# Kernel tuning notes

Measured on AMD Instinct MI355X. Metric: run time of the kernel, lower is better.

The kernel has to match this reference:

```python
import jax, jax.numpy as jnp
import numpy as np

B = 16384       # batch
H = 512         # hidden_size
OUT = 4         # output_size (== GRU input_size)
FF = 2048       # MLP hidden width
HORIZON = 5     # prediction_horizon


def setup_inputs() -> dict:
    key = jax.random.key(0)
    ks = jax.random.split(key, 12)
    s = 0.05
    f32 = jnp.float32
    return {
        "predicted_values": jax.random.normal(ks[0], (B, HORIZON, OUT), f32),
        "past_time_features": jax.random.normal(ks[1], (B, H), f32),
        # nn.GRU (single layer) params, PyTorch layout: (3H, in) / (3H, H), gate order r,z,n
        "w_ih": jax.random.normal(ks[2], (3 * H, OUT), f32) * s,
        "w_hh": jax.random.normal(ks[3], (3 * H, H), f32) * s,
        "b_ih": jax.random.normal(ks[4], (3 * H,), f32) * s,
        "b_hh": jax.random.normal(ks[5], (3 * H,), f32) * s,
        # hx_fc: Linear(2H -> H)
        "w_fc": jax.random.normal(ks[6], (H, 2 * H), f32) * s,
        "b_fc": jax.random.normal(ks[7], (H,), f32) * s,
        # mlp: Linear(H -> 2048), Linear(2048 -> OUT); Dropout is identity at eval
        "w1": jax.random.normal(ks[8], (FF, H), f32) * s,
        "b1": jax.random.normal(ks[9], (FF,), f32) * s,
        "w2": jax.random.normal(ks[10], (OUT, FF), f32) * s,
        "b2": jax.random.normal(ks[11], (OUT,), f32) * s,
    }


def _gru_cell(x, h, w_ih, w_hh, b_ih, b_hh):
    # PyTorch GRU cell: gates ordered (r, z, n)
    gi = x @ w_ih.T + b_ih          # [B, 3H]
    gh = h @ w_hh.T + b_hh          # [B, 3H]
    i_r, i_z, i_n = jnp.split(gi, 3, axis=-1)
    h_r, h_z, h_n = jnp.split(gh, 3, axis=-1)
    r = jax.nn.sigmoid(i_r + h_r)
    z = jax.nn.sigmoid(i_z + h_z)
    n = jnp.tanh(i_n + r * h_n)
    return (1.0 - z) * n + z * h


def reference(predicted_values, past_time_features, w_ih, w_hh, b_ih, b_hh,
              w_fc, b_fc, w1, b1, w2, b2):
    b = predicted_values.shape[0]
    xy = jnp.zeros((b, OUT), predicted_values.dtype)
    hx = past_time_features.reshape(b, H)
    outs = []
    for i in range(HORIZON):
        # length-2 sequence through the GRU: [xy, predicted_values[:, i]]
        h1 = _gru_cell(xy, hx, w_ih, w_hh, b_ih, b_hh)
        h2 = _gru_cell(predicted_values[:, i, :], h1, w_ih, w_hh, b_ih, b_hh)
        hcat = jnp.concatenate([h1, h2], axis=-1)        # [B, 2H]
        hx = hcat @ w_fc.T + b_fc                        # [B, H]
        # MLP: ReLU -> Linear -> (Dropout=identity) -> ReLU -> Linear
        d_xy = jax.nn.relu(jax.nn.relu(hx) @ w1.T + b1) @ w2.T + b2
        xy = xy + d_xy
        outs.append(xy)
    return jnp.stack(outs, axis=1)                       # [B, HORIZON, OUT]
```

## Files before the change

### kernel.cpp

```cpp
#include <hip/hip_runtime.h>
#include <hip/hip_bf16.h>
#include <cstdint>
#include <cstddef>

#define Bsz 16384
#define HORsz 5

using bf16_t = __hip_bfloat16;
typedef __bf16 bf16x8 __attribute__((ext_vector_type(8)));
typedef float f32x4 __attribute__((ext_vector_type(4)));

__device__ __forceinline__ void gld_lds16(const void* g, void* l) {
  __builtin_amdgcn_global_load_lds((__attribute__((address_space(1))) void*)g,
                                   (__attribute__((address_space(3))) void*)l,
                                   16, 0, 0);
}

__device__ __forceinline__ float sigm(float x) { return 1.f / (1.f + __expf(-x)); }
__device__ __forceinline__ float tanh_fast(float x) {
  x = fminf(fmaxf(x, -20.f), 20.f);
  float e = __expf(2.f * x);
  return (e - 1.f) / (e + 1.f);
}

__device__ __forceinline__ void swz(int b, int nbn, int& n, int& m) {
  const int x = b & 7;
  const int k = b >> 3;
  n = k % nbn;
  m = x + 8 * (k / nbn);
}

__device__ __forceinline__ size_t fl_off(int row, int col, int ca, int cofs) {
  return (size_t)((row >> 4) * ca + cofs + (col >> 5)) * 1024
       + (size_t)((((col >> 3) & 3) * 16 + (row & 15)) * 16 + (col & 7) * 2);
}

__global__ void __launch_bounds__(256) pack_fl(const float* __restrict__ src,
                                               char* __restrict__ dst,
                                               int C, int cs, int npieces) {
  const int p = blockIdx.x * 256 + threadIdx.x;
  if (p >= npieces) return;
  const int chunk = p >> 6, wi = p & 63;
  const int colgrp = wi >> 4, r15 = wi & 15;
  const int rowgrp = chunk >> cs, kg = chunk & ((1 << cs) - 1);
  const int row = rowgrp * 16 + r15;
  const int col = kg * 32 + colgrp * 8;
  const float* s = src + (size_t)row * C + col;
  bf16x8 v;
  #pragma unroll
  for (int j = 0; j < 8; ++j) v[j] = (__bf16)s[j];
  *(bf16x8*)(dst + (size_t)p * 16) = v;
}

__global__ void __launch_bounds__(256, 3) gru_fused4(
    const char* __restrict__ Afl, int ca,
    const char* __restrict__ Wfl,
    const float* __restrict__ x, int ldx,
    const float* __restrict__ w_ih, const float* __restrict__ b_ih,
    const float* __restrict__ b_hh,
    char* __restrict__ Ofl, int co, int kofs)
{
  __shared__ char smem[32768];
  const int t = threadIdx.x, w = t >> 6, lane = t & 63;
  int bn, bm;
  swz(blockIdx.x, 8, bn, bm);
  const int m0 = bm * 64;
  const int n0 = bn * 64;

  const char* gsrc[4];
  int loff[4];
  #pragma unroll
  for (int s = 0; s < 4; ++s) {
    const int idx = w * 4 + s;
    if (idx < 4) {
      gsrc[s] = Afl + (size_t)((m0 >> 4) + idx) * ca * 1024 + lane * 16;
    } else {
      const int c = idx - 4, g = c >> 2, cr = c & 3;
      gsrc[s] = Wfl + (size_t)(g * 32 + (n0 >> 4) + cr) * 16 * 1024 + lane * 16;
    }
    loff[s] = idx * 1024;
  }

  f32x4 acc[3][4];
  const f32x4 zero = {0.f, 0.f, 0.f, 0.f};
  #pragma unroll
  for (int g = 0; g < 3; ++g)
    #pragma unroll
    for (int i = 0; i < 4; ++i) acc[g][i] = zero;

  #pragma unroll
  for (int s = 0; s < 4; ++s)
    gld_lds16(gsrc[s], smem + loff[s]);

  #pragma unroll
  for (int kg = 0; kg < 16; ++kg) {
    __syncthreads();
    const char* cur = smem + (kg & 1) * 16384;
    if (kg + 1 < 16) {
      char* nxt = smem + ((kg + 1) & 1) * 16384;
      #pragma unroll
      for (int s = 0; s < 4; ++s)
        gld_lds16(gsrc[s] + (size_t)(kg + 1) * 1024, nxt + loff[s]);
    }
    bf16x8 af[4];
    #pragma unroll
    for (int i = 0; i < 4; ++i)
      af[i] = *(const bf16x8*)(cur + i * 1024 + lane * 16);
    #pragma unroll
    for (int g = 0; g < 3; ++g) {
      const bf16x8 bv = *(const bf16x8*)(cur + (4 + g * 4 + w) * 1024 + lane * 16);
      #pragma unroll
      for (int i = 0; i < 4; ++i)
        acc[g][i] = __builtin_amdgcn_mfma_f32_16x16x32_bf16(af[i], bv, acc[g][i], 0, 0, 0);
    }
  }

  const int lr = lane & 15, q4 = (lane >> 4) * 4;
  char* rep = smem + w * 2048;
  const int c = n0 + w * 16 + lr;
  const float4 wr  = *(const float4*)(w_ih + (size_t)c * 4);
  const float4 wz  = *(const float4*)(w_ih + (size_t)(c + 512) * 4);
  const float4 wnn = *(const float4*)(w_ih + (size_t)(c + 1024) * 4);
  const float bir = b_ih[c], biz = b_ih[c + 512], bin = b_ih[c + 1024];
  const float bhr = b_hh[c], bhz = b_hh[c + 512], bhn = b_hh[c + 1024];
  const int wbase = ((lr >> 3) * 16 + q4) * 16 + (lr & 7) * 2;
  #pragma unroll
  for (int i = 0; i < 4; ++i) {
    #pragma unroll
    for (int r4 = 0; r4 < 4; ++r4) {
      const int row = m0 + i * 16 + q4 + r4;
      const float4 xv = *(const float4*)(x + (size_t)row * ldx);
      const float gir = bir + xv.x * wr.x  + xv.y * wr.y  + xv.z * wr.z  + xv.w * wr.w;
      const float giz = biz + xv.x * wz.x  + xv.y * wz.y  + xv.z * wz.z  + xv.w * wz.w;
      const float gin = bin + xv.x * wnn.x + xv.y * wnn.y + xv.z * wnn.z + xv.w * wnn.w;
      const float rr = sigm(gir + acc[0][i][r4] + bhr);
      const float zz = sigm(giz + acc[1][i][r4] + bhz);
      const float nn = tanh_fast(gin + rr * (acc[2][i][r4] + bhn));
      const float hp = (float)*(const __bf16*)(Afl + fl_off(row, c, ca, 0));
      *(__bf16*)(rep + i * 512 + wbase + r4 * 16) = (__bf16)((1.f - zz) * nn + zz * hp);
    }
  }
  const int rg0 = m0 >> 4;
  const int cg = kofs + (n0 >> 5) + (w >> 1);
  const int half = (w & 1) * 512;
  #pragma unroll
  for (int i = 0; i < 4; ++i) {
    const uint2 v = *(const uint2*)(rep + i * 512 + lane * 8);
    *(uint2*)(Ofl + ((size_t)(rg0 + i) * co + cg) * 1024 + half + lane * 8) = v;
  }
}

template <int NKG, int NJ, int MODE>
__global__ void __launch_bounds__(256, 4) gemm_fl5(
    const char* __restrict__ Afl,
    const char* __restrict__ Bfl, int nbn,
    const float* __restrict__ bias,
    char* __restrict__ O1, char* __restrict__ O2, int co,
    const float* __restrict__ w2, float* __restrict__ dxy)
{
  constexpr int NCH = 8 + 2 * NJ;
  constexpr int NS = NCH / 4;
  constexpr int BUFB = NCH * 1024;
  __shared__ char smem[2 * BUFB];
  const int t = threadIdx.x, w = t >> 6, lane = t & 63;
  int bn, bm;
  swz(blockIdx.x, nbn, bn, bm);
  const int m0 = bm * 128, n0 = bn * (NJ * 32);
  const int wm = (w >> 1) * 64, wn = (w & 1) * (NJ * 16);

  const char* gsrc[NS];
  int loff[NS];
  #pragma unroll
  for (int s = 0; s < NS; ++s) {
    const int idx = w * NS + s;
    if (idx < 8) gsrc[s] = Afl + (size_t)((m0 >> 4) + idx) * NKG * 1024 + lane * 16;
    else         gsrc[s] = Bfl + (size_t)((n0 >> 4) + idx - 8) * NKG * 1024 + lane * 16;
    loff[s] = idx * 1024;
  }

  f32x4 acc[4][NJ];
  const f32x4 zero = {0.f, 0.f, 0.f, 0.f};
  #pragma unroll
  for (int i = 0; i < 4; ++i)
    #pragma unroll
    for (int j = 0; j < NJ; ++j) acc[i][j] = zero;

  #pragma unroll
  for (int s = 0; s < NS; ++s)
    gld_lds16(gsrc[s], smem + loff[s]);

  #pragma unroll
  for (int kg = 0; kg < NKG; ++kg) {
    __syncthreads();
    const char* cur = smem + (kg & 1) * BUFB;
    if (kg + 1 < NKG) {
      char* nxt = smem + ((kg + 1) & 1) * BUFB;
      #pragma unroll
      for (int s = 0; s < NS; ++s)
        gld_lds16(gsrc[s] + (size_t)(kg + 1) * 1024, nxt + loff[s]);
    }
    bf16x8 af[4], bv[NJ];
    #pragma unroll
    for (int i = 0; i < 4; ++i)
      af[i] = *(const bf16x8*)(cur + ((wm >> 4) + i) * 1024 + lane * 16);
    #pragma unroll
    for (int j = 0; j < NJ; ++j)
      bv[j] = *(const bf16x8*)(cur + (8 + (wn >> 4) + j) * 1024 + lane * 16);
    #pragma unroll
    for (int i = 0; i < 4; ++i)
      #pragma unroll
      for (int j = 0; j < NJ; ++j)
        acc[i][j] = __builtin_amdgcn_mfma_f32_16x16x32_bf16(af[i], bv[j], acc[i][j], 0, 0, 0);
  }

  const int lr = lane & 15, q4 = (lane >> 4) * 4;
  if (MODE == 2) {
    char* rep = smem + w * (NJ / 2) * 1024;
    const int rgb = (m0 >> 4) + (wm >> 4);
    const int cgb = (n0 >> 5) + (wn >> 5);
    for (int i = 0; i < 4; ++i) {
      #pragma unroll
      for (int j = 0; j < NJ; ++j) {
        const int col = n0 + wn + j * 16 + lr;
        const float bvv = bias[col];
        const int wbase = (((j & 1) * 2 + (lr >> 3)) * 16 + q4) * 16 + (lr & 7) * 2;
        #pragma unroll
        for (int r = 0; r < 4; ++r) {
          const float v = acc[i][j][r] + bvv;
          *(__bf16*)(rep + (j >> 1) * 1024 + wbase + r * 16) = (__bf16)v;
        }
      }
      #pragma unroll
      for (int jc = 0; jc < NJ / 2; ++jc) {
        const bf16x8 v = *(const bf16x8*)(rep + jc * 1024 + lane * 16);
        const size_t cb = ((size_t)(rgb + i) * co + cgb + jc) * 1024 + lane * 16;
        *(bf16x8*)(O1 + cb) = v;
        bf16x8 vr;
        #pragma unroll
        for (int e = 0; e < 8; ++e) vr[e] = (__bf16)fmaxf((float)v[e], 0.f);
        *(bf16x8*)(O2 + cb) = vr;
      }
    }
  }
}

__global__ void __launch_bounds__(512, 2) mlp2b(
    const char* __restrict__ Afl,
    const char* __restrict__ Bfl,
    const float* __restrict__ bias,
    const float* __restrict__ w2,
    float* __restrict__ dxy)
{
  __shared__ char smem[2 * 32768];
  const int t = threadIdx.x, w = t >> 6, lane = t & 63;
  const int wr = w >> 2, wc = w & 3;
  int bn, bm;
  swz(blockIdx.x, 8, bn, bm);
  const int m0 = bm * 256, n0 = bn * 256;

  const char* gsrc[4];
  int loff[4];
  #pragma unroll
  for (int s = 0; s < 4; ++s) {
    const int idx = w * 4 + s;
    if (idx < 16) {
      gsrc[s] = Afl + (size_t)((m0 >> 4) + idx) * 16 * 1024 + lane * 16;
      loff[s] = idx * 1024;
    } else {
      gsrc[s] = Bfl + (size_t)((n0 >> 4) + idx - 16) * 16 * 1024 + lane * 16;
      loff[s] = 16384 + (idx - 16) * 1024;
    }
  }

  f32x4 acc[8][4];
  const f32x4 zero = {0.f, 0.f, 0.f, 0.f};
  #pragma unroll
  for (int i = 0; i < 8; ++i)
    #pragma unroll
    for (int j = 0; j < 4; ++j) acc[i][j] = zero;

  #pragma unroll
  for (int s = 0; s < 4; ++s)
    gld_lds16(gsrc[s], smem + loff[s]);

  #pragma unroll
  for (int kg = 0; kg < 16; ++kg) {
    __syncthreads();
    const char* cur = smem + (kg & 1) * 32768;
    if (kg + 1 < 16) {
      char* nxt = smem + ((kg + 1) & 1) * 32768;
      #pragma unroll
      for (int s = 0; s < 4; ++s)
        gld_lds16(gsrc[s] + (size_t)(kg + 1) * 1024, nxt + loff[s]);
    }
    bf16x8 af[8], bv[4];
    #pragma unroll
    for (int j = 0; j < 4; ++j)
      bv[j] = *(const bf16x8*)(cur + 16384 + (wc * 4 + j) * 1024 + lane * 16);
    #pragma unroll
    for (int i = 0; i < 8; ++i)
      af[i] = *(const bf16x8*)(cur + (wr * 8 + i) * 1024 + lane * 16);
    __builtin_amdgcn_s_setprio(1);
    #pragma unroll
    for (int i = 0; i < 8; ++i)
      #pragma unroll
      for (int j = 0; j < 4; ++j)
        acc[i][j] = __builtin_amdgcn_mfma_f32_16x16x32_bf16(af[i], bv[j], acc[i][j], 0, 0, 0);
    __builtin_amdgcn_s_setprio(0);
  }

  const int lr = lane & 15, q4 = (lane >> 4) * 4;
  const int slice = bn * 4 + wc;
  #pragma unroll
  for (int i = 0; i < 8; ++i) {
    float v[4][4];
    #pragma unroll
    for (int r = 0; r < 4; ++r)
      #pragma unroll
      for (int o = 0; o < 4; ++o) v[r][o] = 0.f;
    #pragma unroll
    for (int j = 0; j < 4; ++j) {
      const int col = n0 + wc * 64 + j * 16 + lr;
      const float bvv = bias[col];
      const float w20 = w2[col], w21 = w2[2048 + col], w22 = w2[4096 + col], w23 = w2[6144 + col];
      #pragma unroll
      for (int r = 0; r < 4; ++r) {
        const float pv = fmaxf(acc[i][j][r] + bvv, 0.f);
        v[r][0] += pv * w20; v[r][1] += pv * w21; v[r][2] += pv * w22; v[r][3] += pv * w23;
      }
    }
    #pragma unroll
    for (int m = 1; m <= 8; m <<= 1)
      #pragma unroll
      for (int r = 0; r < 4; ++r)
        #pragma unroll
        for (int o = 0; o < 4; ++o) v[r][o] += __shfl_xor(v[r][o], m);
    if (lr == 0) {
      #pragma unroll
      for (int r = 0; r < 4; ++r) {
        const int row = m0 + wr * 128 + i * 16 + q4 + r;
        float4 vv = make_float4(v[r][0], v[r][1], v[r][2], v[r][3]);
        *(float4*)(dxy + ((size_t)slice * Bsz + row) * 4) = vv;
      }
    }
  }
}

__global__ void __launch_bounds__(256) finalize(
    const float* __restrict__ dxy, const float* __restrict__ b2,
    float* __restrict__ xy, float* __restrict__ out, int istep)
{
  const int b = blockIdx.x * 256 + threadIdx.x;
  float4 s = *(const float4*)b2;
  #pragma unroll 8
  for (int sl = 0; sl < 32; ++sl) {
    const float4 d = *(const float4*)(dxy + ((size_t)sl * Bsz + b) * 4);
    s.x += d.x; s.y += d.y; s.z += d.z; s.w += d.w;
  }
  float4 xv = *(const float4*)(xy + (size_t)b * 4);
  xv.x += s.x; xv.y += s.y; xv.z += s.z; xv.w += s.w;
  *(float4*)(xy + (size_t)b * 4) = xv;
  *(float4*)(out + (size_t)b * 20 + istep * 4) = xv;
}

extern "C" void kernel_launch(void* const* d_in, const int* in_sizes, int n_in,
                              void* d_out, int out_size, void* d_ws, size_t ws_size,
                              hipStream_t stream)
{
  const float* pv   = (const float*)d_in[0];
  const float* ptf  = (const float*)d_in[1];
  const float* w_ih = (const float*)d_in[2];
  const float* w_hh = (const float*)d_in[3];
  const float* b_ih = (const float*)d_in[4];
  const float* b_hh = (const float*)d_in[5];
  const float* w_fc = (const float*)d_in[6];
  const float* b_fc = (const float*)d_in[7];
  const float* w1   = (const float*)d_in[8];
  const float* b1   = (const float*)d_in[9];
  const float* w2   = (const float*)d_in[10];
  const float* b2   = (const float*)d_in[11];
  float* out = (float*)d_out;

  char* p = (char*)d_ws;
  auto carve = [&](size_t bytes) {
    char* r = p;
    p += (bytes + 255) & ~(size_t)255;
    return r;
  };
  char*  hxF   = carve((size_t)Bsz * 512 * 2);
  char*  hxrF  = carve((size_t)Bsz * 512 * 2);
  char*  hcatF = carve((size_t)Bsz * 1024 * 2);
  float* dxy   = (float*)carve((size_t)32 * Bsz * 4 * 4);
  float* xy    = (float*)carve((size_t)Bsz * 4 * 4);
  char*  whhF  = carve((size_t)1536 * 512 * 2);
  char*  wfcF  = carve((size_t)512 * 1024 * 2);
  char*  w1F   = carve((size_t)2048 * 512 * 2);

  pack_fl<<<(1536 * 512 / 8 + 255) / 256, 256, 0, stream>>>(w_hh, whhF, 512, 4, 1536 * 512 / 8);
  pack_fl<<<(512 * 1024 / 8 + 255) / 256, 256, 0, stream>>>(w_fc, wfcF, 1024, 5, 512 * 1024 / 8);
  pack_fl<<<(2048 * 512 / 8 + 255) / 256, 256, 0, stream>>>(w1, w1F, 512, 4, 2048 * 512 / 8);
  pack_fl<<<(Bsz * 512 / 8 + 255) / 256, 256, 0, stream>>>(ptf, hxF, 512, 4, Bsz * 512 / 8);
  hipMemsetAsync(xy, 0, (size_t)Bsz * 4 * 4, stream);

  for (int i = 0; i < HORsz; ++i) {
    gru_fused4<<<2048, 256, 0, stream>>>(
        hxF, 16, whhF, xy, 4, w_ih, b_ih, b_hh, hcatF, 32, 0);
    gru_fused4<<<2048, 256, 0, stream>>>(
        hcatF, 32, whhF, pv + i * 4, HORsz * 4, w_ih, b_ih, b_hh, hcatF, 32, 16);
    gemm_fl5<32, 4, 2><<<512, 256, 0, stream>>>(
        hcatF, wfcF, 4, b_fc, hxF, hxrF, 16, nullptr, nullptr);
    mlp2b<<<512, 512, 0, stream>>>(hxrF, w1F, b1, w2, dxy);
    finalize<<<Bsz / 256, 256, 0, stream>>>(dxy, b2, xy, out, i);
  }
}
```

Baseline: 876.5 us.

## Double GRU tile rows to 128, hoist MLP epilogue loads, use DPP reductions

The GRU kernel tile grows from 64 to 128 batch rows per block, so each W_hh chunk loaded into shared memory feeds twice as many MFMAs. The grid is halved, shared memory and accumulator registers grow, and launch bounds drop to 2 blocks per SM. In the MLP epilogue, bias and w2 loads are hoisted out of the row loop. The 16-lane shuffle reduction is replaced with DPP adds. The risk is lower occupancy and register pressure in the GRU kernel.

```diff
diff --git a/kernel.cpp b/kernel.cpp
--- a/kernel.cpp
+++ b/kernel.cpp
@@ -21,6 +21,19 @@
   x = fminf(fmaxf(x, -20.f), 20.f);
   float e = __expf(2.f * x);
   return (e - 1.f) / (e + 1.f);
+}
+
+template <int CTRL>
+__device__ __forceinline__ float dpp_add(float v) {
+  int x = __builtin_amdgcn_update_dpp(0, __float_as_int(v), CTRL, 0xF, 0xF, true);
+  return v + __int_as_float(x);
+}
+__device__ __forceinline__ float red16(float v) {
+  v = dpp_add<0xB1>(v);
+  v = dpp_add<0x4E>(v);
+  v = dpp_add<0x124>(v);
+  v = dpp_add<0x128>(v);
+  return v;
 }
 
 __device__ __forceinline__ void swz(int b, int nbn, int& n, int& m) {
@@ -52,7 +65,7 @@
   *(bf16x8*)(dst + (size_t)p * 16) = v;
 }
 
-__global__ void __launch_bounds__(256, 3) gru_fused4(
+__global__ void __launch_bounds__(256, 2) gru_fused8(
     const char* __restrict__ Afl, int ca,
     const char* __restrict__ Wfl,
     const float* __restrict__ x, int ldx,
@@ -60,63 +73,63 @@
     const float* __restrict__ b_hh,
     char* __restrict__ Ofl, int co, int kofs)
 {
-  __shared__ char smem[32768];
+  __shared__ char smem[40960];
   const int t = threadIdx.x, w = t >> 6, lane = t & 63;
   int bn, bm;
   swz(blockIdx.x, 8, bn, bm);
-  const int m0 = bm * 64;
+  const int m0 = bm * 128;
   const int n0 = bn * 64;
 
-  const char* gsrc[4];
-  int loff[4];
-  #pragma unroll
-  for (int s = 0; s < 4; ++s) {
-    const int idx = w * 4 + s;
-    if (idx < 4) {
+  const char* gsrc[5];
+  int loff[5];
+  #pragma unroll
+  for (int s = 0; s < 5; ++s) {
+    const int idx = w * 5 + s;
+    if (idx < 8) {
       gsrc[s] = Afl + (size_t)((m0 >> 4) + idx) * ca * 1024 + lane * 16;
     } else {
-      const int c = idx - 4, g = c >> 2, cr = c & 3;
+      const int c = idx - 8, g = c >> 2, cr = c & 3;
       gsrc[s] = Wfl + (size_t)(g * 32 + (n0 >> 4) + cr) * 16 * 1024 + lane * 16;
     }
     loff[s] = idx * 1024;
   }
 
-  f32x4 acc[3][4];
+  f32x4 acc[3][8];
   const f32x4 zero = {0.f, 0.f, 0.f, 0.f};
   #pragma unroll
   for (int g = 0; g < 3; ++g)
     #pragma unroll
-    for (int i = 0; i < 4; ++i) acc[g][i] = zero;
-
-  #pragma unroll
-  for (int s = 0; s < 4; ++s)
+    for (int i = 0; i < 8; ++i) acc[g][i] = zero;
+
+  #pragma unroll
+  for (int s = 0; s < 5; ++s)
     gld_lds16(gsrc[s], smem + loff[s]);
 
   #pragma unroll
   for (int kg = 0; kg < 16; ++kg) {
     __syncthreads();
-    const char* cur = smem + (kg & 1) * 16384;
+    const char* cur = smem + (kg & 1) * 20480;
     if (kg + 1 < 16) {
-      char* nxt = smem + ((kg + 1) & 1) * 16384;
-      #pragma unroll
-      for (int s = 0; s < 4; ++s)
+      char* nxt = smem + ((kg + 1) & 1) * 20480;
+      #pragma unroll
+      for (int s = 0; s < 5; ++s)
         gld_lds16(gsrc[s] + (size_t)(kg + 1) * 1024, nxt + loff[s]);
     }
-    bf16x8 af[4];
-    #pragma unroll
-    for (int i = 0; i < 4; ++i)
+    bf16x8 af[8];
+    #pragma unroll
+    for (int i = 0; i < 8; ++i)
       af[i] = *(const bf16x8*)(cur + i * 1024 + lane * 16);
     #pragma unroll
     for (int g = 0; g < 3; ++g) {
-      const bf16x8 bv = *(const bf16x8*)(cur + (4 + g * 4 + w) * 1024 + lane * 16);
-      #pragma unroll
-      for (int i = 0; i < 4; ++i)
+      const bf16x8 bv = *(const bf16x8*)(cur + 8192 + (g * 4 + w) * 1024 + lane * 16);
+      #pragma unroll
+      for (int i = 0; i < 8; ++i)
         acc[g][i] = __builtin_amdgcn_mfma_f32_16x16x32_bf16(af[i], bv, acc[g][i], 0, 0, 0);
     }
   }
 
   const int lr = lane & 15, q4 = (lane >> 4) * 4;
-  char* rep = smem + w * 2048;
+  char* rep = smem + w * 4096;
   const int c = n0 + w * 16 + lr;
   const float4 wr  = *(const float4*)(w_ih + (size_t)c * 4);
   const float4 wz  = *(const float4*)(w_ih + (size_t)(c + 512) * 4);
@@ -125,7 +138,7 @@
   const float bhr = b_hh[c], bhz = b_hh[c + 512], bhn = b_hh[c + 1024];
   const int wbase = ((lr >> 3) * 16 + q4) * 16 + (lr & 7) * 2;
   #pragma unroll
-  for (int i = 0; i < 4; ++i) {
+  for (int i = 0; i < 8; ++i) {
     #pragma unroll
     for (int r4 = 0; r4 < 4; ++r4) {
       const int row = m0 + i * 16 + q4 + r4;
@@ -144,7 +157,7 @@
   const int cg = kofs + (n0 >> 5) + (w >> 1);
   const int half = (w & 1) * 512;
   #pragma unroll
-  for (int i = 0; i < 4; ++i) {
+  for (int i = 0; i < 8; ++i) {
     const uint2 v = *(const uint2*)(rep + i * 512 + lane * 8);
     *(uint2*)(Ofl + ((size_t)(rg0 + i) * co + cg) * 1024 + half + lane * 8) = v;
   }
@@ -311,6 +324,14 @@
 
   const int lr = lane & 15, q4 = (lane >> 4) * 4;
   const int slice = bn * 4 + wc;
+  float bvv[4], w2c[4][4];
+  #pragma unroll
+  for (int j = 0; j < 4; ++j) {
+    const int col = n0 + wc * 64 + j * 16 + lr;
+    bvv[j] = bias[col];
+    w2c[j][0] = w2[col];        w2c[j][1] = w2[2048 + col];
+    w2c[j][2] = w2[4096 + col]; w2c[j][3] = w2[6144 + col];
+  }
   #pragma unroll
   for (int i = 0; i < 8; ++i) {
     float v[4][4];
@@ -320,21 +341,17 @@
       for (int o = 0; o < 4; ++o) v[r][o] = 0.f;
     #pragma unroll
     for (int j = 0; j < 4; ++j) {
-      const int col = n0 + wc * 64 + j * 16 + lr;
-      const float bvv = bias[col];
-      const float w20 = w2[col], w21 = w2[2048 + col], w22 = w2[4096 + col], w23 = w2[6144 + col];
       #pragma unroll
       for (int r = 0; r < 4; ++r) {
-        const float pv = fmaxf(acc[i][j][r] + bvv, 0.f);
-        v[r][0] += pv * w20; v[r][1] += pv * w21; v[r][2] += pv * w22; v[r][3] += pv * w23;
+        const float pv = fmaxf(acc[i][j][r] + bvv[j], 0.f);
+        v[r][0] += pv * w2c[j][0]; v[r][1] += pv * w2c[j][1];
+        v[r][2] += pv * w2c[j][2]; v[r][3] += pv * w2c[j][3];
       }
     }
     #pragma unroll
-    for (int m = 1; m <= 8; m <<= 1)
-      #pragma unroll
-      for (int r = 0; r < 4; ++r)
-        #pragma unroll
-        for (int o = 0; o < 4; ++o) v[r][o] += __shfl_xor(v[r][o], m);
+    for (int r = 0; r < 4; ++r)
+      #pragma unroll
+      for (int o = 0; o < 4; ++o) v[r][o] = red16(v[r][o]);
     if (lr == 0) {
       #pragma unroll
       for (int r = 0; r < 4; ++r) {
@@ -403,9 +420,9 @@
   hipMemsetAsync(xy, 0, (size_t)Bsz * 4 * 4, stream);
 
   for (int i = 0; i < HORsz; ++i) {
-    gru_fused4<<<2048, 256, 0, stream>>>(
+    gru_fused8<<<1024, 256, 0, stream>>>(
         hxF, 16, whhF, xy, 4, w_ih, b_ih, b_hh, hcatF, 32, 0);
-    gru_fused4<<<2048, 256, 0, stream>>>(
+    gru_fused8<<<1024, 256, 0, stream>>>(
         hcatF, 32, whhF, pv + i * 4, HORsz * 4, w_ih, b_ih, b_hh, hcatF, 32, 16);
     gemm_fl5<32, 4, 2><<<512, 256, 0, stream>>>(
         hcatF, wfcF, 4, b_fc, hxF, hxrF, 16, nullptr, nullptr);
```

New measurement: 872.3 us. About the same (-0.5%).
